# Performance work log

Measured on AMD Instinct MI355X. Metric: run time of the kernel, lower is better.

Reference implementation:

```python
import jax, jax.numpy as jnp
import numpy as np

BITS = 4
MAXQ = (1 << BITS) - 1
PACK = 32 // BITS  # values packed per int32
GROUP_SIZE = 128


def dequant_weight(qweight, qzeros, scales, g_idx):
    """GPTQ tritonv2-style dequant: W[i,j] = (w_int[i,j] - z_int[g_idx[i],j]) * scales[g_idx[i],j]."""
    in_features = qweight.shape[0] * PACK
    out_features = qweight.shape[1]
    rows = jnp.arange(in_features)
    # unpack along infeatures: row i lives in qweight[i//PACK], nibble (i%PACK)
    w_int = (qweight[rows // PACK] >> ((rows % PACK) * BITS)[:, None]) & MAXQ  # [in, out]
    cols = jnp.arange(out_features)
    # unpack zeros along outfeatures
    z_int = (qzeros[:, cols // PACK] >> ((cols % PACK) * BITS)[None, :]) & MAXQ  # [groups, out]
    dt = scales.dtype
    return (w_int.astype(dt) - z_int.astype(dt)[g_idx]) * scales[g_idx]  # [in, out]


def setup_inputs() -> dict:
    key = jax.random.key(0)
    k1, k2, k3, k4, k5 = jax.random.split(key, 5)
    B, S, IN, OUT = 4, 2048, 4096, 11008
    groups = IN // GROUP_SIZE
    x = jax.random.normal(k1, (B, S, IN), dtype=jnp.float32)
    qweight = jax.random.randint(k2, (IN // PACK, OUT), 0, 2147483647, dtype=jnp.int32)
    qzeros = jax.random.randint(k3, (groups, OUT // PACK), 0, 2147483647, dtype=jnp.int32)
    scales = jax.random.uniform(k4, (groups, OUT), dtype=jnp.float32, minval=0.001, maxval=0.02)
    g_idx = (jnp.arange(IN) // GROUP_SIZE).astype(jnp.int32)
    bias = jax.random.normal(k5, (OUT,), dtype=jnp.float32) * 0.01
    return {"x": x, "qweight": qweight, "qzeros": qzeros, "scales": scales, "g_idx": g_idx, "bias": bias}


def reference(x, qweight, qzeros, scales, g_idx, bias):
    W = dequant_weight(qweight, qzeros, scales, g_idx)  # [in, out]
    out = x.reshape(-1, x.shape[-1]) @ W + bias  # [tokens, out]
    return out.reshape(x.shape[:-1] + (W.shape[1],)).astype(x.dtype)
```

## Files before the change

kernel.cpp:

```cpp
#include <hip/hip_runtime.h>

typedef __bf16 bf16x8 __attribute__((ext_vector_type(8)));
typedef __bf16 bf16x4 __attribute__((ext_vector_type(4)));
typedef float  f32x4  __attribute__((ext_vector_type(4)));

typedef __attribute__((address_space(3))) unsigned int        lds_u32_t;
typedef const __attribute__((address_space(1))) unsigned int  glob_u32_t;

__global__ __launch_bounds__(256)
void cvt_x_bf16(const float* __restrict__ X, __bf16* __restrict__ XB, long long n8)
{
    long long i = (long long)blockIdx.x * 256 + threadIdx.x;
    if (i >= n8) return;
    const float4* src = (const float4*)X + 2 * i;
    float4 a = src[0], b = src[1];
    bf16x8 v = { (__bf16)a.x, (__bf16)a.y, (__bf16)a.z, (__bf16)a.w,
                 (__bf16)b.x, (__bf16)b.y, (__bf16)b.z, (__bf16)b.w };
    *(bf16x8*)(XB + 8 * i) = v;
}

__global__ __launch_bounds__(256)
void dequant_wt(const unsigned int* __restrict__ QW,
                const unsigned int* __restrict__ QZ,
                const float* __restrict__ SC,
                __bf16* __restrict__ WT,
                const int N, const int K)
{
    __shared__ __bf16 T[256 * 64];
    const int tid = threadIdx.x;
    const int nK  = K >> 6;
    const int n0  = (blockIdx.x / nK) * 256;
    const int k0  = (blockIdx.x % nK) * 64;

    const int n = n0 + tid;
    const int g = k0 >> 7;
    const float s = SC[g * N + n];
    const unsigned int qzv = QZ[g * (N >> 3) + (n >> 3)];
    const float nz = (float)((qzv >> ((n & 7) * 4)) & 15) * s;
    const int qr0 = k0 >> 3;

    #pragma unroll
    for (int i = 0; i < 8; ++i) {
        const unsigned int w32 = QW[(size_t)(qr0 + i) * N + n];
        bf16x8 v;
        #pragma unroll
        for (int j = 0; j < 8; ++j)
            v[j] = (__bf16)((float)((w32 >> (4 * j)) & 15) * s - nz);
        *(bf16x8*)((char*)T + tid * 128 + ((i ^ (tid & 7)) << 4)) = v;
    }
    __syncthreads();
    #pragma unroll
    for (int it = 0; it < 8; ++it) {
        const int r = it * 32 + (tid >> 3);
        const int c = tid & 7;
        bf16x8 v = *(bf16x8*)((char*)T + r * 128 + ((c ^ (r & 7)) << 4));
        *(bf16x8*)(WT + (size_t)(n0 + r) * K + k0 + c * 8) = v;
    }
}

__global__ __launch_bounds__(256, 2)
void gemm_bt_bf16(const __bf16* __restrict__ A,
                  const __bf16* __restrict__ B,
                  const float* __restrict__ BIAS,
                  float* __restrict__ OUT,
                  const int M, const int N, const int K)
{
    __shared__ __bf16 As[128 * 64];
    __shared__ __bf16 Bs[128 * 64];

    const int tid  = threadIdx.x;
    const int lane = tid & 63;
    const int wave = tid >> 6;

    const int cpx = gridDim.x >> 3;
    int bid = blockIdx.x;
    bid = (bid & 7) * cpx + (bid >> 3);

    const int nTn = N >> 7;
    const int m0  = (bid / nTn) << 7;
    const int n0  = (bid % nTn) << 7;

    const int wm  = (wave >> 1) * 64;
    const int wn  = (wave & 1) * 64;
    const int l15 = lane & 15;
    const int lhi = lane >> 4;

    f32x4 acc[4][4] = {};

    const size_t abase = (size_t)m0 * K;
    const size_t bbase = (size_t)n0 * K;

    const int kTiles = K >> 6;
    for (int kt = 0; kt < kTiles; ++kt) {
        const int k0 = kt << 6;
        __syncthreads();
        #pragma unroll
        for (int i = 0; i < 4; ++i) {
            const int c   = tid + 256 * i;
            const int row = c >> 3;
            const int sc_ = (c & 7) ^ (row & 7);
            __builtin_amdgcn_global_load_lds(
                (glob_u32_t*)(A + abase + (size_t)row * K + k0 + sc_ * 8),
                (lds_u32_t*)((char*)As + c * 16), 16, 0, 0);
            __builtin_amdgcn_global_load_lds(
                (glob_u32_t*)(B + bbase + (size_t)row * K + k0 + sc_ * 8),
                (lds_u32_t*)((char*)Bs + c * 16), 16, 0, 0);
        }
        __syncthreads();

        #pragma unroll
        for (int ks = 0; ks < 2; ++ks) {
            bf16x8 af[4], bfr[4];
            #pragma unroll
            for (int mi = 0; mi < 4; ++mi) {
                const int row = wm + mi * 16 + l15;
                const int ch  = (ks * 4 + lhi) ^ (row & 7);
                af[mi] = *(bf16x8*)((char*)As + row * 128 + (ch << 4));
            }
            #pragma unroll
            for (int ni = 0; ni < 4; ++ni) {
                const int row = wn + ni * 16 + l15;
                const int ch  = (ks * 4 + lhi) ^ (row & 7);
                bfr[ni] = *(bf16x8*)((char*)Bs + row * 128 + (ch << 4));
            }
            #pragma unroll
            for (int mi = 0; mi < 4; ++mi)
                #pragma unroll
                for (int ni = 0; ni < 4; ++ni)
                    acc[mi][ni] = __builtin_amdgcn_mfma_f32_16x16x32_bf16(
                        af[mi], bfr[ni], acc[mi][ni], 0, 0, 0);
        }
    }

    const int cb = n0 + wn + l15;
    const int rb = m0 + wm + (lane >> 4) * 4;
    #pragma unroll
    for (int ni = 0; ni < 4; ++ni) {
        const float bv = BIAS[cb + ni * 16];
        #pragma unroll
        for (int mi = 0; mi < 4; ++mi)
            #pragma unroll
            for (int r = 0; r < 4; ++r)
                OUT[(size_t)(rb + mi * 16 + r) * N + cb + ni * 16] = acc[mi][ni][r] + bv;
    }
}

constexpr int BM  = 128;
constexpr int BN  = 128;
constexpr int BK  = 64;
constexpr int LDK = 72;

__global__ __launch_bounds__(256, 2)
void gptq_gemm_fused(const float* __restrict__ X,
                     const unsigned int* __restrict__ QW,
                     const unsigned int* __restrict__ QZ,
                     const float* __restrict__ SC,
                     const float* __restrict__ BIAS,
                     float* __restrict__ OUT,
                     const int M, const int N, const int K)
{
    __shared__ __bf16 As[BM * LDK];
    __shared__ __bf16 Bs[BN * LDK];

    const int tid = threadIdx.x;
    const int nTn = N / BN;
    const int m0  = (blockIdx.x / nTn) * BM;
    const int n0  = (blockIdx.x % nTn) * BN;

    const int lane = tid & 63;
    const int wave = tid >> 6;
    const int wm   = (wave >> 1) * 64;
    const int wn   = (wave & 1) * 64;
    const int l15  = lane & 15;
    const int lk8  = (lane >> 4) * 8;

    const int a_kc = (tid & 15) * 4;
    const int a_r0 = tid >> 4;
    const int b_c  = tid & 127;
    const int b_r0 = tid >> 7;
    const int N8   = N >> 3;

    f32x4 acc[4][4] = {};
    float4 av[8];
    unsigned int bw[4];
    float scale, nzs;

    auto load_tile = [&](int kt_) {
        const int k0 = kt_ * BK;
        #pragma unroll
        for (int i = 0; i < 8; ++i)
            av[i] = *(const float4*)&X[(m0 + a_r0 + 16 * i) * K + k0 + a_kc];
        const int qr = k0 >> 3;
        #pragma unroll
        for (int i = 0; i < 4; ++i)
            bw[i] = QW[(qr + b_r0 + 2 * i) * N + n0 + b_c];
        const int g = k0 >> 7;
        scale = SC[g * N + n0 + b_c];
        const unsigned int qzv = QZ[g * N8 + ((n0 + b_c) >> 3)];
        const int z = (qzv >> (((n0 + b_c) & 7) * 4)) & 15;
        nzs = (float)z * scale;
    };

    load_tile(0);

    const int kTiles = K / BK;
    for (int kt = 0; kt < kTiles; ++kt) {
        __syncthreads();
        #pragma unroll
        for (int i = 0; i < 8; ++i) {
            bf16x4 v = { (__bf16)av[i].x, (__bf16)av[i].y,
                         (__bf16)av[i].z, (__bf16)av[i].w };
            *(bf16x4*)&As[(a_r0 + 16 * i) * LDK + a_kc] = v;
        }
        {
            const float s = scale, nz = nzs;
            #pragma unroll
            for (int i = 0; i < 4; ++i) {
                const unsigned int w32 = bw[i];
                bf16x8 v;
                #pragma unroll
                for (int j = 0; j < 8; ++j) {
                    const int w = (w32 >> (4 * j)) & 15;
                    v[j] = (__bf16)((float)w * s - nz);
                }
                *(bf16x8*)&Bs[b_c * LDK + (b_r0 + 2 * i) * 8] = v;
            }
        }
        __syncthreads();

        if (kt + 1 < kTiles) load_tile(kt + 1);

        #pragma unroll
        for (int ks = 0; ks < 2; ++ks) {
            bf16x8 af[4], bfr[4];
            #pragma unroll
            for (int mi = 0; mi < 4; ++mi)
                af[mi] = *(bf16x8*)&As[(wm + mi * 16 + l15) * LDK + ks * 32 + lk8];
            #pragma unroll
            for (int ni = 0; ni < 4; ++ni)
                bfr[ni] = *(bf16x8*)&Bs[(wn + ni * 16 + l15) * LDK + ks * 32 + lk8];
            #pragma unroll
            for (int mi = 0; mi < 4; ++mi)
                #pragma unroll
                for (int ni = 0; ni < 4; ++ni)
                    acc[mi][ni] = __builtin_amdgcn_mfma_f32_16x16x32_bf16(
                        af[mi], bfr[ni], acc[mi][ni], 0, 0, 0);
        }
    }

    const int cb = n0 + wn + l15;
    const int rb = m0 + wm + (lane >> 4) * 4;
    #pragma unroll
    for (int ni = 0; ni < 4; ++ni) {
        const float bv = BIAS[cb + ni * 16];
        #pragma unroll
        for (int mi = 0; mi < 4; ++mi)
            #pragma unroll
            for (int r = 0; r < 4; ++r)
                OUT[(size_t)(rb + mi * 16 + r) * N + cb + ni * 16] = acc[mi][ni][r] + bv;
    }
}

extern "C" void kernel_launch(void* const* d_in, const int* in_sizes, int n_in,
                              void* d_out, int out_size, void* d_ws, size_t ws_size,
                              hipStream_t stream) {
    const float*        x    = (const float*)d_in[0];
    const unsigned int* qw   = (const unsigned int*)d_in[1];
    const unsigned int* qz   = (const unsigned int*)d_in[2];
    const float*        sc   = (const float*)d_in[3];
    const float*        bias = (const float*)d_in[5];
    float*              out  = (float*)d_out;

    const int K = in_sizes[4];
    const int N = in_sizes[5];
    const int M = in_sizes[0] / K;

    const size_t needA = (size_t)M * K * 2;
    const size_t needB = (size_t)N * K * 2;
    const int    nwg   = (M / 128) * (N / 128);
    const bool canSplit = (ws_size >= needA + needB) &&
                          (M % 128 == 0) && (N % 256 == 0) && (K % 128 == 0) &&
                          ((nwg & 7) == 0);

    if (canSplit) {
        __bf16* xb = (__bf16*)d_ws;
        __bf16* wt = (__bf16*)((char*)d_ws + needA);
        const long long n8 = (long long)M * K / 8;
        cvt_x_bf16<<<(int)((n8 + 255) / 256), 256, 0, stream>>>(x, xb, n8);
        dequant_wt<<<(N / 256) * (K / 64), 256, 0, stream>>>(qw, qz, sc, wt, N, K);
        gemm_bt_bf16<<<nwg, 256, 0, stream>>>(xb, wt, bias, out, M, N, K);
    } else {
        gptq_gemm_fused<<<nwg, 256, 0, stream>>>(x, qw, qz, sc, bias, out, M, N, K);
    }
}
```

Baseline: 1.306 ms.

## Replace 128x128 bf16 GEMM with double-buffered 256x256 phased-pipeline kernel

The bf16 GEMM now computes 256x256 output tiles with 512 threads (8 waves) instead of 128x128 tiles with 256 threads. It uses 128KB of dynamic LDS as two buffers, so global-to-LDS loads for the next K tile are issued in quarters between MFMA phases. Phases are coordinated with explicit vmcnt/lgkmcnt waits, barriers and setprio. The goal is to raise arithmetic intensity per byte loaded and to hide load latency behind matrix math. In exchange, occupancy drops to one block per CU, register pressure rises from the 8x4 accumulators, and the split path now requires M to be a multiple of 256.

After: 1.107 ms. 1.18x faster.

```diff
diff --git a/kernel.cpp b/kernel.cpp
--- a/kernel.cpp
+++ b/kernel.cpp
@@ -58,15 +58,45 @@
     }
 }
 
-__global__ __launch_bounds__(256, 2)
-void gemm_bt_bf16(const __bf16* __restrict__ A,
-                  const __bf16* __restrict__ B,
-                  const float* __restrict__ BIAS,
-                  float* __restrict__ OUT,
-                  const int M, const int N, const int K)
+
+#define PH_READS(b, ks, mh)                                                        \
+  {                                                                                \
+    if ((mh) == 0) {                                                               \
+      _Pragma("unroll")                                                            \
+      for (int ni = 0; ni < 4; ++ni)                                               \
+        bfr[ni] = *(const bf16x8*)(smem + 65536 + (b) * 32768 +                    \
+                     (wnRow + ni * 16 + l15) * 128 + ((((ks)*4 + lhi) ^ l7) << 4));\
+    }                                                                              \
+    _Pragma("unroll")                                                              \
+    for (int mi = 0; mi < 4; ++mi)                                                 \
+      af[mi] = *(const bf16x8*)(smem + (b) * 32768 +                               \
+                 (wmRow + ((mh)*4 + mi) * 16 + l15) * 128 +                        \
+                 ((((ks)*4 + lhi) ^ l7) << 4));                                    \
+  }
+
+#define PH_MFMA(mh)                                                                \
+  {                                                                                \
+    asm volatile("s_waitcnt lgkmcnt(0)" ::: "memory");                             \
+    __builtin_amdgcn_sched_barrier(0);                                             \
+    __builtin_amdgcn_s_setprio(1);                                                 \
+    _Pragma("unroll")                                                              \
+    for (int mi = 0; mi < 4; ++mi)                                                 \
+      _Pragma("unroll")                                                            \
+      for (int ni = 0; ni < 4; ++ni)                                               \
+        acc[(mh)*4 + mi][ni] = __builtin_amdgcn_mfma_f32_16x16x32_bf16(            \
+            af[mi], bfr[ni], acc[(mh)*4 + mi][ni], 0, 0, 0);                       \
+    __builtin_amdgcn_s_setprio(0);                                                 \
+    __builtin_amdgcn_s_barrier();                                                  \
+  }
+
+__global__ __launch_bounds__(512, 2)
+void gemm_bt_256(const __bf16* __restrict__ A,
+                 const __bf16* __restrict__ B,
+                 const float* __restrict__ BIAS,
+                 float* __restrict__ OUT,
+                 const int M, const int N, const int K)
 {
-    __shared__ __bf16 As[128 * 64];
-    __shared__ __bf16 Bs[128 * 64];
+    extern __shared__ char smem[];
 
     const int tid  = threadIdx.x;
     const int lane = tid & 63;
@@ -76,69 +106,95 @@
     int bid = blockIdx.x;
     bid = (bid & 7) * cpx + (bid >> 3);
 
-    const int nTn = N >> 7;
-    const int m0  = (bid / nTn) << 7;
-    const int n0  = (bid % nTn) << 7;
-
-    const int wm  = (wave >> 1) * 64;
-    const int wn  = (wave & 1) * 64;
-    const int l15 = lane & 15;
-    const int lhi = lane >> 4;
-
-    f32x4 acc[4][4] = {};
-
-    const size_t abase = (size_t)m0 * K;
-    const size_t bbase = (size_t)n0 * K;
-
-    const int kTiles = K >> 6;
-    for (int kt = 0; kt < kTiles; ++kt) {
-        const int k0 = kt << 6;
-        __syncthreads();
-        #pragma unroll
-        for (int i = 0; i < 4; ++i) {
-            const int c   = tid + 256 * i;
+    const int nTn = N >> 8;
+    const int m0  = (bid / nTn) << 8;
+    const int n0  = (bid % nTn) << 8;
+
+    const int wmRow = (wave >> 2) * 128;
+    const int wnRow = (wave & 3) * 64;
+    const int l15   = lane & 15;
+    const int lhi   = lane >> 4;
+    const int l7    = l15 & 7;
+
+    f32x4 acc[8][4] = {};
+    bf16x8 af[4], bfr[4];
+
+    const size_t Ks = (size_t)K;
+
+    auto stage_half = [&](const __bf16* src, int gRow0, int t, int ldsBase) {
+        const size_t base = (size_t)gRow0 * Ks + (size_t)t * 64;
+        #pragma unroll
+        for (int j = 0; j < 2; ++j) {
+            const int c   = tid + 512 * j;
             const int row = c >> 3;
-            const int sc_ = (c & 7) ^ (row & 7);
+            const int sc  = (c & 7) ^ (row & 7);
             __builtin_amdgcn_global_load_lds(
-                (glob_u32_t*)(A + abase + (size_t)row * K + k0 + sc_ * 8),
-                (lds_u32_t*)((char*)As + c * 16), 16, 0, 0);
-            __builtin_amdgcn_global_load_lds(
-                (glob_u32_t*)(B + bbase + (size_t)row * K + k0 + sc_ * 8),
-                (lds_u32_t*)((char*)Bs + c * 16), 16, 0, 0);
-        }
-        __syncthreads();
-
-        #pragma unroll
-        for (int ks = 0; ks < 2; ++ks) {
-            bf16x8 af[4], bfr[4];
-            #pragma unroll
-            for (int mi = 0; mi < 4; ++mi) {
-                const int row = wm + mi * 16 + l15;
-                const int ch  = (ks * 4 + lhi) ^ (row & 7);
-                af[mi] = *(bf16x8*)((char*)As + row * 128 + (ch << 4));
-            }
-            #pragma unroll
-            for (int ni = 0; ni < 4; ++ni) {
-                const int row = wn + ni * 16 + l15;
-                const int ch  = (ks * 4 + lhi) ^ (row & 7);
-                bfr[ni] = *(bf16x8*)((char*)Bs + row * 128 + (ch << 4));
-            }
-            #pragma unroll
-            for (int mi = 0; mi < 4; ++mi)
-                #pragma unroll
-                for (int ni = 0; ni < 4; ++ni)
-                    acc[mi][ni] = __builtin_amdgcn_mfma_f32_16x16x32_bf16(
-                        af[mi], bfr[ni], acc[mi][ni], 0, 0, 0);
-        }
-    }
-
-    const int cb = n0 + wn + l15;
-    const int rb = m0 + wm + (lane >> 4) * 4;
+                (glob_u32_t*)(src + base + (size_t)row * Ks + sc * 8),
+                (lds_u32_t*)(smem + ldsBase + c * 16), 16, 0, 0);
+        }
+    };
+    auto stage_tile_half = [&](int t, int hh, int b) {
+        if (hh < 2) stage_half(A, m0 + hh * 128, t, b * 32768 + hh * 16384);
+        else        stage_half(B, n0 + (hh - 2) * 128, t,
+                               65536 + b * 32768 + (hh - 2) * 16384);
+    };
+
+    #pragma unroll
+    for (int hh = 0; hh < 4; ++hh) stage_tile_half(0, hh, 0);
+
+    const int kT    = K >> 6;
+    const int nIter = kT >> 1;
+
+    for (int i = 0; i < nIter; ++i) {
+        const int t1   = 2 * i + 1;
+        const int t2   = 2 * i + 2;
+        const bool more = (t2 < kT);
+
+        stage_tile_half(t1, 0, 1);
+        asm volatile("s_waitcnt vmcnt(2)" ::: "memory");
+        __builtin_amdgcn_s_barrier();
+        PH_READS(0, 0, 0); PH_MFMA(0);
+        PH_READS(0, 0, 1);
+        stage_tile_half(t1, 1, 1);
+        __builtin_amdgcn_s_barrier();
+        PH_MFMA(1);
+        PH_READS(0, 1, 0);
+        stage_tile_half(t1, 2, 1);
+        __builtin_amdgcn_s_barrier();
+        PH_MFMA(0);
+        PH_READS(0, 1, 1);
+        stage_tile_half(t1, 3, 1);
+        __builtin_amdgcn_s_barrier();
+        PH_MFMA(1);
+        if (more) {
+            stage_tile_half(t2, 0, 0);
+            asm volatile("s_waitcnt vmcnt(2)" ::: "memory");
+        } else {
+            asm volatile("s_waitcnt vmcnt(0)" ::: "memory");
+        }
+        __builtin_amdgcn_s_barrier();
+        PH_READS(1, 0, 0); PH_MFMA(0);
+        PH_READS(1, 0, 1);
+        if (more) stage_tile_half(t2, 1, 0);
+        __builtin_amdgcn_s_barrier();
+        PH_MFMA(1);
+        PH_READS(1, 1, 0);
+        if (more) stage_tile_half(t2, 2, 0);
+        __builtin_amdgcn_s_barrier();
+        PH_MFMA(0);
+        PH_READS(1, 1, 1);
+        if (more) stage_tile_half(t2, 3, 0);
+        __builtin_amdgcn_s_barrier();
+        PH_MFMA(1);
+    }
+
+    const int cb = n0 + wnRow + l15;
+    const int rb = m0 + wmRow + (lane >> 4) * 4;
     #pragma unroll
     for (int ni = 0; ni < 4; ++ni) {
         const float bv = BIAS[cb + ni * 16];
         #pragma unroll
-        for (int mi = 0; mi < 4; ++mi)
+        for (int mi = 0; mi < 8; ++mi)
             #pragma unroll
             for (int r = 0; r < 4; ++r)
                 OUT[(size_t)(rb + mi * 16 + r) * N + cb + ni * 16] = acc[mi][ni][r] + bv;
@@ -277,9 +333,9 @@
 
     const size_t needA = (size_t)M * K * 2;
     const size_t needB = (size_t)N * K * 2;
-    const int    nwg   = (M / 128) * (N / 128);
+    const int    nwg   = (M / 256) * (N / 256);
     const bool canSplit = (ws_size >= needA + needB) &&
-                          (M % 128 == 0) && (N % 256 == 0) && (K % 128 == 0) &&
+                          (M % 256 == 0) && (N % 256 == 0) && (K % 128 == 0) &&
                           ((nwg & 7) == 0);
 
     if (canSplit) {
@@ -288,8 +344,11 @@
         const long long n8 = (long long)M * K / 8;
         cvt_x_bf16<<<(int)((n8 + 255) / 256), 256, 0, stream>>>(x, xb, n8);
         dequant_wt<<<(N / 256) * (K / 64), 256, 0, stream>>>(qw, qz, sc, wt, N, K);
-        gemm_bt_bf16<<<nwg, 256, 0, stream>>>(xb, wt, bias, out, M, N, K);
+        (void)hipFuncSetAttribute((const void*)gemm_bt_256,
+                                  hipFuncAttributeMaxDynamicSharedMemorySize, 131072);
+        gemm_bt_256<<<nwg, 512, 131072, stream>>>(xb, wt, bias, out, M, N, K);
     } else {
-        gptq_gemm_fused<<<nwg, 256, 0, stream>>>(x, qw, qz, sc, bias, out, M, N, K);
-    }
-}
+        const int nwg128 = (M / 128) * (N / 128);
+        gptq_gemm_fused<<<nwg128, 256, 0, stream>>>(x, qw, qz, sc, bias, out, M, N, K);
+    }
+}
```

## Replace bf16 GEMM with 256x256 tile, 512-thread double-buffered pipelined kernel

Applied to the files above, without the earlier changes.

Replaces the 128x128 single-buffered GEMM with a 256x256 tile kernel run by 8 waves. It uses 128 KB of dynamic LDS, double buffered and split into half-K stages, with async global-to-LDS loads issued between MFMA phases. The loads are controlled by explicit vmcnt waits, barriers and setprio. The aim is to hide global load latency behind MFMA work and raise arithmetic intensity per tile. In exchange it costs higher register and LDS pressure, a fixed wait-count schedule that depends on the load counts, and stricter shape requirements.

Result: faster. 1.181 ms (-9.6%).

```diff
diff --git a/kernel.cpp b/kernel.cpp
--- a/kernel.cpp
+++ b/kernel.cpp
@@ -58,15 +58,88 @@
     }
 }
 
-__global__ __launch_bounds__(256, 2)
-void gemm_bt_bf16(const __bf16* __restrict__ A,
-                  const __bf16* __restrict__ B,
-                  const float* __restrict__ BIAS,
-                  float* __restrict__ OUT,
-                  const int M, const int N, const int K)
+
+#define RD_A(b_, ks, mh)                                                          \
+  { _Pragma("unroll")                                                             \
+    for (int mi = 0; mi < 4; ++mi) {                                              \
+      const int r = wmRow + ((mh) * 4 + mi) * 16 + l15;                           \
+      af[mi] = *(const bf16x8*)(smem + (b_) * 32768 + (ks) * 16384 + r * 64 +     \
+                                (swz << 4));                                      \
+    } }
+
+#define RD_B(b_, ks)                                                              \
+  { _Pragma("unroll")                                                             \
+    for (int ni = 0; ni < 4; ++ni) {                                              \
+      const int r = wnRow + ni * 16 + l15;                                        \
+      bfr[ni] = *(const bf16x8*)(smem + 65536 + (b_) * 32768 + (ks) * 16384 +     \
+                                 r * 64 + (swz << 4));                            \
+    } }
+
+#define PH_MFMA(mh)                                                               \
+  {                                                                               \
+    asm volatile("s_waitcnt lgkmcnt(0)" ::: "memory");                            \
+    __builtin_amdgcn_sched_barrier(0);                                            \
+    __builtin_amdgcn_s_setprio(1);                                                \
+    _Pragma("unroll")                                                             \
+    for (int mi = 0; mi < 4; ++mi)                                                \
+      _Pragma("unroll")                                                           \
+      for (int ni = 0; ni < 4; ++ni)                                              \
+        acc[(mh) * 4 + mi][ni] = __builtin_amdgcn_mfma_f32_16x16x32_bf16(         \
+            af[mi], bfr[ni], acc[(mh) * 4 + mi][ni], 0, 0, 0);                    \
+    __builtin_amdgcn_s_setprio(0);                                                \
+    __builtin_amdgcn_s_barrier();                                                 \
+  }
+
+#define STG_A(t, h)                                                               \
+  { _Pragma("unroll")                                                             \
+    for (int j = 0; j < 2; ++j)                                                   \
+      __builtin_amdgcn_global_load_lds(                                           \
+          (glob_u32_t*)(A + aOff[j] + (size_t)((t) * 64 + (h) * 32)),             \
+          (lds_u32_t*)(smem + ((t) & 1) * 32768 + (h) * 16384 + ldsC[j]),         \
+          16, 0, 0); }
+#define STG_B(t, h)                                                               \
+  { _Pragma("unroll")                                                             \
+    for (int j = 0; j < 2; ++j)                                                   \
+      __builtin_amdgcn_global_load_lds(                                           \
+          (glob_u32_t*)(B + bOff[j] + (size_t)((t) * 64 + (h) * 32)),             \
+          (lds_u32_t*)(smem + 65536 + ((t) & 1) * 32768 + (h) * 16384 + ldsC[j]), \
+          16, 0, 0); }
+
+#define EPOCH(T, S1, S2, W0, W2)                                                  \
+  {                                                                               \
+    const int b_ = (T) & 1;                                                       \
+                            \
+    if (S1) STG_A((T) + 1, 1);                                                    \
+    asm volatile("s_waitcnt vmcnt(" W0 ")" ::: "memory");                         \
+    __builtin_amdgcn_s_barrier();                                                 \
+    RD_B(b_, 0); RD_A(b_, 0, 0);                                                  \
+    PH_MFMA(0);                                                                   \
+                            \
+    RD_A(b_, 0, 1);                                                               \
+    if (S1) STG_B((T) + 1, 1);                                                    \
+    __builtin_amdgcn_s_barrier();                                                 \
+    PH_MFMA(1);                                                                   \
+                            \
+    if (S2) STG_A((T) + 2, 0);                                                    \
+    asm volatile("s_waitcnt vmcnt(" W2 ")" ::: "memory");                         \
+    __builtin_amdgcn_s_barrier();                                                 \
+    RD_B(b_, 1); RD_A(b_, 1, 0);                                                  \
+    PH_MFMA(0);                                                                   \
+                            \
+    RD_A(b_, 1, 1);                                                               \
+    if (S2) STG_B((T) + 2, 0);                                                    \
+    __builtin_amdgcn_s_barrier();                                                 \
+    PH_MFMA(1);                                                                   \
+  }
+
+__global__ __launch_bounds__(512)
+void gemm_bt_256(const __bf16* __restrict__ A,
+                 const __bf16* __restrict__ B,
+                 const float* __restrict__ BIAS,
+                 float* __restrict__ OUT,
+                 const int M, const int N, const int K)
 {
-    __shared__ __bf16 As[128 * 64];
-    __shared__ __bf16 Bs[128 * 64];
+    extern __shared__ char smem[];
 
     const int tid  = threadIdx.x;
     const int lane = tid & 63;
@@ -76,69 +149,46 @@
     int bid = blockIdx.x;
     bid = (bid & 7) * cpx + (bid >> 3);
 
-    const int nTn = N >> 7;
-    const int m0  = (bid / nTn) << 7;
-    const int n0  = (bid % nTn) << 7;
-
-    const int wm  = (wave >> 1) * 64;
-    const int wn  = (wave & 1) * 64;
-    const int l15 = lane & 15;
-    const int lhi = lane >> 4;
-
-    f32x4 acc[4][4] = {};
-
-    const size_t abase = (size_t)m0 * K;
-    const size_t bbase = (size_t)n0 * K;
-
-    const int kTiles = K >> 6;
-    for (int kt = 0; kt < kTiles; ++kt) {
-        const int k0 = kt << 6;
-        __syncthreads();
-        #pragma unroll
-        for (int i = 0; i < 4; ++i) {
-            const int c   = tid + 256 * i;
-            const int row = c >> 3;
-            const int sc_ = (c & 7) ^ (row & 7);
-            __builtin_amdgcn_global_load_lds(
-                (glob_u32_t*)(A + abase + (size_t)row * K + k0 + sc_ * 8),
-                (lds_u32_t*)((char*)As + c * 16), 16, 0, 0);
-            __builtin_amdgcn_global_load_lds(
-                (glob_u32_t*)(B + bbase + (size_t)row * K + k0 + sc_ * 8),
-                (lds_u32_t*)((char*)Bs + c * 16), 16, 0, 0);
-        }
-        __syncthreads();
-
-        #pragma unroll
-        for (int ks = 0; ks < 2; ++ks) {
-            bf16x8 af[4], bfr[4];
-            #pragma unroll
-            for (int mi = 0; mi < 4; ++mi) {
-                const int row = wm + mi * 16 + l15;
-                const int ch  = (ks * 4 + lhi) ^ (row & 7);
-                af[mi] = *(bf16x8*)((char*)As + row * 128 + (ch << 4));
-            }
-            #pragma unroll
-            for (int ni = 0; ni < 4; ++ni) {
-                const int row = wn + ni * 16 + l15;
-                const int ch  = (ks * 4 + lhi) ^ (row & 7);
-                bfr[ni] = *(bf16x8*)((char*)Bs + row * 128 + (ch << 4));
-            }
-            #pragma unroll
-            for (int mi = 0; mi < 4; ++mi)
-                #pragma unroll
-                for (int ni = 0; ni < 4; ++ni)
-                    acc[mi][ni] = __builtin_amdgcn_mfma_f32_16x16x32_bf16(
-                        af[mi], bfr[ni], acc[mi][ni], 0, 0, 0);
-        }
-    }
-
-    const int cb = n0 + wn + l15;
-    const int rb = m0 + wm + (lane >> 4) * 4;
+    const int nTn = N >> 8;
+    const int m0  = (bid / nTn) << 8;
+    const int n0  = (bid % nTn) << 8;
+
+    const int wmRow = (wave >> 2) * 128;
+    const int wnRow = (wave & 3) * 64;
+    const int l15   = lane & 15;
+    const int lhi   = lane >> 4;
+    const int swz   = lhi ^ (l15 & 3);
+
+    f32x4 acc[8][4] = {};
+    bf16x8 af[4], bfr[4];
+
+    size_t aOff[2], bOff[2];
+    int ldsC[2];
+    #pragma unroll
+    for (int j = 0; j < 2; ++j) {
+        const int c   = tid + 512 * j;
+        const int row = c >> 2;
+        const int scc = (c & 3) ^ (row & 3);
+        aOff[j] = (size_t)(m0 + row) * K + scc * 8;
+        bOff[j] = (size_t)(n0 + row) * K + scc * 8;
+        ldsC[j] = c * 16;
+    }
+
+    STG_A(0, 0); STG_B(0, 0); STG_A(0, 1); STG_B(0, 1); STG_A(1, 0); STG_B(1, 0);
+
+    const int kT = K >> 6;
+    int t = 0;
+    for (; t < kT - 2; ++t) EPOCH(t, true, true, "10", "10");
+    EPOCH(t, true, false, "10", "8");  ++t;
+    EPOCH(t, false, false, "4", "0");
+
+    const int cb = n0 + wnRow + l15;
+    const int rb = m0 + wmRow + (lane >> 4) * 4;
     #pragma unroll
     for (int ni = 0; ni < 4; ++ni) {
         const float bv = BIAS[cb + ni * 16];
         #pragma unroll
-        for (int mi = 0; mi < 4; ++mi)
+        for (int mi = 0; mi < 8; ++mi)
             #pragma unroll
             for (int r = 0; r < 4; ++r)
                 OUT[(size_t)(rb + mi * 16 + r) * N + cb + ni * 16] = acc[mi][ni][r] + bv;
@@ -277,10 +327,10 @@
 
     const size_t needA = (size_t)M * K * 2;
     const size_t needB = (size_t)N * K * 2;
-    const int    nwg   = (M / 128) * (N / 128);
+    const int    nwg   = (M / 256) * (N / 256);
     const bool canSplit = (ws_size >= needA + needB) &&
-                          (M % 128 == 0) && (N % 256 == 0) && (K % 128 == 0) &&
-                          ((nwg & 7) == 0);
+                          (M % 256 == 0) && (N % 256 == 0) && (K % 128 == 0) &&
+                          (K >= 256) && ((nwg & 7) == 0);
 
     if (canSplit) {
         __bf16* xb = (__bf16*)d_ws;
@@ -288,8 +338,11 @@
         const long long n8 = (long long)M * K / 8;
         cvt_x_bf16<<<(int)((n8 + 255) / 256), 256, 0, stream>>>(x, xb, n8);
         dequant_wt<<<(N / 256) * (K / 64), 256, 0, stream>>>(qw, qz, sc, wt, N, K);
-        gemm_bt_bf16<<<nwg, 256, 0, stream>>>(xb, wt, bias, out, M, N, K);
+        (void)hipFuncSetAttribute((const void*)gemm_bt_256,
+                                  hipFuncAttributeMaxDynamicSharedMemorySize, 131072);
+        gemm_bt_256<<<nwg, 512, 131072, stream>>>(xb, wt, bias, out, M, N, K);
     } else {
-        gptq_gemm_fused<<<nwg, 256, 0, stream>>>(x, qw, qz, sc, bias, out, M, N, K);
-    }
-}
+        const int nwg128 = (M / 128) * (N / 128);
+        gptq_gemm_fused<<<nwg128, 256, 0, stream>>>(x, qw, qz, sc, bias, out, M, N, K);
+    }
+}
```
